# Performance work log

Measured on AMD Instinct MI355X. Metric: run time of the kernel, lower is better.

## Reference

```python
import jax, jax.numpy as jnp
import numpy as np

N, E, H, L = 50000, 600000, 128, 4  # nodes, edges, hidden_dim, num_layers


def setup_inputs() -> dict:
    key = jax.random.key(0)
    ks = jax.random.split(key, 12)
    def w(k, shape):
        fan_in = shape[-2]
        return jax.random.normal(k, shape, jnp.float32) / np.float32(np.sqrt(fan_in))
    return {
        "loc": jax.random.normal(ks[0], (N, 3), jnp.float32),
        "vel": jax.random.normal(ks[1], (N, 3), jnp.float32),
        "edge_attr": jax.random.normal(ks[2], (E, 2), jnp.float32),
        "row": jax.random.randint(ks[3], (E,), 0, N),
        "col": jax.random.randint(ks[4], (E,), 0, N),
        # embedding: Linear(6 -> H)
        "emb_w": w(ks[5], (6, H)), "emb_b": jnp.zeros((H,), jnp.float32),
        # per-layer edge MLP: Linear(2H+2 -> H), SiLU, Linear(H -> H), SiLU
        "ew1": w(ks[6], (L, 2 * H + 2, H)), "eb1": jnp.zeros((L, H), jnp.float32),
        "ew2": w(ks[7], (L, H, H)), "eb2": jnp.zeros((L, H), jnp.float32),
        # per-layer node MLP: Linear(2H -> H), SiLU, Linear(H -> H)
        "nw1": w(ks[8], (L, 2 * H, H)), "nb1": jnp.zeros((L, H), jnp.float32),
        "nw2": w(ks[9], (L, H, H)), "nb2": jnp.zeros((L, H), jnp.float32),
        # decoder: Linear(H -> H), SiLU, Linear(H -> 3)
        "dw1": w(ks[10], (H, H)), "db1": jnp.zeros((H,), jnp.float32),
        "dw2": w(ks[11], (H, 3)), "db2": jnp.zeros((3,), jnp.float32),
    }


def reference(loc, vel, edge_attr, row, col, emb_w, emb_b, ew1, eb1, ew2, eb2,
              nw1, nb1, nw2, nb2, dw1, db1, dw2, db2):
    silu = jax.nn.silu
    # embedding of [loc, vel]
    h = jnp.concatenate([loc, vel], axis=1) @ emb_w + emb_b  # [N, H]
    for i in range(L):
        # edge model: gather endpoints, concat edge_attr, 2-layer SiLU MLP
        e_in = jnp.concatenate([h[row], h[col], edge_attr], axis=1)  # [E, 2H+2]
        m = silu(silu(e_in @ ew1[i] + eb1[i]) @ ew2[i] + eb2[i])     # [E, H]
        # node model: scatter-sum messages into source nodes (row), MLP, residual
        agg = jax.ops.segment_sum(m, row, num_segments=N)            # [N, H]
        upd = silu(jnp.concatenate([h, agg], axis=1) @ nw1[i] + nb1[i]) @ nw2[i] + nb2[i]
        h = h + upd  # recurrent=True
    return silu(h @ dw1 + db1) @ dw2 + db2  # [N, 3]
```

## Files before the change

kernel.cpp:

```cpp
#include <hip/hip_runtime.h>

#define NN 50000
#define NE 600000
#define HD 128
#define NL 4
#define NSCB 196
#define NWG_E (NE/64)

typedef __bf16 bf16x8 __attribute__((ext_vector_type(8)));
typedef float f32x4 __attribute__((ext_vector_type(4)));

__device__ __forceinline__ unsigned short f2bf(float x){
  union { float f; unsigned int u; } v; v.f = x;
  unsigned int r = v.u + 0x7FFFu + ((v.u >> 16) & 1u);
  return (unsigned short)(r >> 16);
}
__device__ __forceinline__ float silu_f(float x){
  float e, r;
  float t = x * -1.44269504088896340736f;
  asm("v_exp_f32 %0, %1" : "=v"(e) : "v"(t));
  float d = 1.f + e;
  asm("v_rcp_f32 %0, %1" : "=v"(r) : "v"(d));
  return x * r;
}
__device__ __forceinline__ unsigned pk_bf16(float v0, float v1){
  unsigned r;
  asm("v_cvt_pk_bf16_f32 %0, %1, %2" : "=v"(r) : "v"(v0), "v"(v1));
  return r;
}
__device__ __forceinline__ void atomic_pk_add_bf16(unsigned short* addr, unsigned data){
  asm volatile("global_atomic_pk_add_bf16 %0, %1, off"
    :: "v"((unsigned long long)(uintptr_t)addr), "v"(data) : "memory");
}

__device__ __forceinline__ f32x4 mfma_b16(bf16x8 a, bf16x8 b, f32x4 c){
  return __builtin_amdgcn_mfma_f32_16x16x32_bf16(a, b, c, 0, 0, 0);
}

typedef __attribute__((address_space(1))) const unsigned int* gas1p;
typedef __attribute__((address_space(3))) unsigned int* las3p;
__device__ __forceinline__ void gll16(const void* g, void* l){
  __builtin_amdgcn_global_load_lds((gas1p)g, (las3p)l, 16, 0, 0);
}

__global__ __launch_bounds__(256) void pack_b(const float* __restrict__ src,
    unsigned short* __restrict__ dst, int K, int Klimit, int srcLayerStride, int perm){
  int layer = blockIdx.y;
  int tid = blockIdx.x*256 + threadIdx.x;
  int j = tid & 7, lane = (tid >> 3) & 63, nb = (tid >> 9) & 7, kk = tid >> 12;
  int krow = (kk << 5) + ((lane >> 4) << 3) + j;
  int ll = lane & 15;
  int c = perm ? (((((nb >> 1) << 4) + ll) << 1) + (nb & 1)) : ((nb << 4) + ll);
  float v = (krow < Klimit) ? src[(size_t)layer*srcLayerStride + krow*HD + c] : 0.f;
  dst[(size_t)layer*K*HD + tid] = f2bf(v);
}

__global__ __launch_bounds__(256) void emb_kernel(
    const float* __restrict__ loc, const float* __restrict__ vel,
    const float* __restrict__ ew, const float* __restrict__ eb,
    float* __restrict__ hf, unsigned short* __restrict__ hb)
{
  int gid = blockIdx.x*256 + threadIdx.x;
  int n = gid >> 7, j = gid & 127;
  float s = eb[j];
  s += loc[n*3+0]*ew[0*HD+j] + loc[n*3+1]*ew[1*HD+j] + loc[n*3+2]*ew[2*HD+j];
  s += vel[n*3+0]*ew[3*HD+j] + vel[n*3+1]*ew[4*HD+j] + vel[n*3+2]*ew[5*HD+j];
  hf[gid] = s;
  hb[gid] = f2bf(s);
}

__global__ __launch_bounds__(256) void count_kernel(const int* __restrict__ rowIdx, int* __restrict__ cnt){
  int e = blockIdx.x*256 + threadIdx.x;
  if (e < NE) atomicAdd(cnt + rowIdx[e], 1);
}

__global__ __launch_bounds__(256) void blocksum_kernel(const int* __restrict__ cnt, int* __restrict__ bsum){
  __shared__ int s[256];
  int t = threadIdx.x, i = blockIdx.x*256 + t;
  s[t] = (i < NN) ? cnt[i] : 0;
  __syncthreads();
  for (int d = 128; d > 0; d >>= 1){
    if (t < d) s[t] += s[t + d];
    __syncthreads();
  }
  if (t == 0) bsum[blockIdx.x] = s[0];
}

__global__ __launch_bounds__(256) void scanb_kernel(int* __restrict__ bsum){
  __shared__ int s[256];
  int t = threadIdx.x;
  int v = (t < NSCB) ? bsum[t] : 0;
  s[t] = v;
  __syncthreads();
  for (int d = 1; d < 256; d <<= 1){
    int u = (t >= d) ? s[t-d] : 0;
    __syncthreads();
    s[t] += u;
    __syncthreads();
  }
  if (t < NSCB) bsum[t] = s[t] - v;
}

__global__ __launch_bounds__(256) void offsets_kernel(const int* __restrict__ cnt,
    const int* __restrict__ bsum, int* __restrict__ cur){
  __shared__ int s[256];
  int t = threadIdx.x, i = blockIdx.x*256 + t;
  int v = (i < NN) ? cnt[i] : 0;
  s[t] = v;
  __syncthreads();
  for (int d = 1; d < 256; d <<= 1){
    int u = (t >= d) ? s[t-d] : 0;
    __syncthreads();
    s[t] += u;
    __syncthreads();
  }
  if (i < NN) cur[i] = bsum[blockIdx.x] + s[t] - v;
}

__global__ __launch_bounds__(256) void assign_kernel(
    const int* __restrict__ rowIdx, const int* __restrict__ colIdx,
    const float* __restrict__ ea, int* __restrict__ cur,
    int* __restrict__ row_s, int* __restrict__ col_s, float* __restrict__ ea_s){
  int e = blockIdx.x*256 + threadIdx.x;
  if (e < NE){
    int r = rowIdx[e];
    int s = atomicAdd(cur + r, 1);
    int s64 = s & 63;
    int sp = (s & ~63) | (((s64 >> 2) & 3) << 4) | (((s64 >> 4) & 3) << 2) | (s64 & 3);
    row_s[sp] = r;
    col_s[sp] = colIdx[e];
    ea_s[2*sp]   = ea[2*e];
    ea_s[2*sp+1] = ea[2*e+1];
  }
}

#define SWZ(a) ((a) ^ (((a) >> 4) & 0x30))

__global__ __launch_bounds__(256, 8) void edge_kernel(
    const unsigned short* __restrict__ hb,
    const int* __restrict__ row_s, const int* __restrict__ col_s,
    const float* __restrict__ ea_s,
    const unsigned short* __restrict__ B1p, const unsigned short* __restrict__ B2p,
    const float* __restrict__ bias1, const float* __restrict__ bias2,
    const float* __restrict__ wea,
    unsigned short* __restrict__ aggb)
{
  __shared__ alignas(128) char sA[1024*16];
  __shared__ int sRow[64];
  __shared__ float2 sEa[64];
  uint4* sA4 = reinterpret_cast<uint4*>(sA);

  const int t = threadIdx.x;
  const int w = t >> 6, l = t & 63, lw = l >> 4, ll = l & 15;

  int orig = blockIdx.x;
  int xcd = orig & 7, idx = orig >> 3;
  const int qq = NWG_E >> 3, rr = NWG_E & 7;
  int bid = (xcd < rr) ? xcd*(qq + 1) + idx : rr*(qq + 1) + (xcd - rr)*qq + idx;
  const int e0 = bid << 6;

  if (t < 64){
    sRow[t] = row_s[e0 + t];
    sEa[t] = reinterpret_cast<const float2*>(ea_s)[e0 + t];
  }
  const int er = e0 + (w << 4) + ll;
  const int nrow = row_s[er];
  const int ncol = col_s[er];
  const unsigned short* gr = hb + (size_t)nrow*HD + (lw << 3);
  #pragma unroll
  for (int kk = 0; kk < 4; ++kk)
    gll16(gr + (kk << 5), sA + ((size_t)(((kk << 2) + w)) << 10));
  asm volatile("s_waitcnt vmcnt(0)" ::: "memory");
  __syncthreads();

  const int q2 = ((w << 4) + ll) << 1;
  const float2 bb1 = *reinterpret_cast<const float2*>(bias1 + q2);
  const float2 wA = *reinterpret_cast<const float2*>(wea + q2);
  const float2 wB = *reinterpret_cast<const float2*>(wea + HD + q2);

  f32x4 acc[4][2] = {};
  #pragma unroll
  for (int kk = 0; kk < 4; ++kk){
    bf16x8 a[4], b[2];
    #pragma unroll
    for (int r = 0; r < 4; ++r)
      a[r] = *reinterpret_cast<const bf16x8*>(&sA4[((kk << 2) + r)*64 + l]);
    #pragma unroll
    for (int c = 0; c < 2; ++c)
      b[c] = *reinterpret_cast<const bf16x8*>(B1p + ((((kk << 3) + (w << 1) + c) << 6) + l)*8);
    #pragma unroll
    for (int r = 0; r < 4; ++r)
      #pragma unroll
      for (int c = 0; c < 2; ++c)
        acc[r][c] = mfma_b16(a[r], b[c], acc[r][c]);
  }
  __syncthreads();

  const unsigned short* gc = hb + (size_t)ncol*HD + (lw << 3);
  #pragma unroll
  for (int kk = 0; kk < 4; ++kk)
    gll16(gc + (kk << 5), sA + ((size_t)(((kk << 2) + w)) << 10));
  asm volatile("s_waitcnt vmcnt(0)" ::: "memory");
  __syncthreads();

  #pragma unroll
  for (int kk = 4; kk < 8; ++kk){
    bf16x8 a[4], b[2];
    #pragma unroll
    for (int r = 0; r < 4; ++r)
      a[r] = *reinterpret_cast<const bf16x8*>(&sA4[(((kk - 4) << 2) + r)*64 + l]);
    #pragma unroll
    for (int c = 0; c < 2; ++c)
      b[c] = *reinterpret_cast<const bf16x8*>(B1p + ((((kk << 3) + (w << 1) + c) << 6) + l)*8);
    #pragma unroll
    for (int r = 0; r < 4; ++r)
      #pragma unroll
      for (int c = 0; c < 2; ++c)
        acc[r][c] = mfma_b16(a[r], b[c], acc[r][c]);
  }
  __syncthreads();

  #pragma unroll
  for (int r = 0; r < 4; ++r){
    #pragma unroll
    for (int i = 0; i < 4; ++i){
      int rt = (r << 4) + (lw << 2) + i;
      float2 eav = sEa[rt];
      float v0 = silu_f(acc[r][0][i] + bb1.x + eav.x*wA.x + eav.y*wB.x);
      float v1 = silu_f(acc[r][1][i] + bb1.y + eav.x*wA.y + eav.y*wB.y);
      unsigned d = pk_bf16(v0, v1);
      int a0 = ((((w << 2) + r) << 10) | ((ll >> 2) << 8) | (lw << 6) | (i << 4) | ((ll & 3) << 2));
      *reinterpret_cast<unsigned*>(sA + SWZ(a0)) = d;
    }
  }
  __syncthreads();

  f32x4 acc2[4][2] = {};
  #pragma unroll
  for (int kk = 0; kk < 4; ++kk){
    bf16x8 a[4], b[2];
    #pragma unroll
    for (int r = 0; r < 4; ++r){
      int a0 = ((((kk << 2) + r) << 10) | (l << 4));
      a[r] = *reinterpret_cast<const bf16x8*>(sA + SWZ(a0));
    }
    #pragma unroll
    for (int c = 0; c < 2; ++c)
      b[c] = *reinterpret_cast<const bf16x8*>(B2p + ((((kk << 3) + (w << 1) + c) << 6) + l)*8);
    #pragma unroll
    for (int r = 0; r < 4; ++r)
      #pragma unroll
      for (int c = 0; c < 2; ++c)
        acc2[r][c] = mfma_b16(a[r], b[c], acc2[r][c]);
  }

  {
    const float2 bb2 = *reinterpret_cast<const float2*>(bias2 + q2);
    int curNode = -1;
    float s0 = 0.f, s1 = 0.f;
    #pragma unroll
    for (int r = 0; r < 4; ++r){
      #pragma unroll
      for (int i = 0; i < 4; ++i){
        int rt = (r << 4) + (lw << 2) + i;
        int nd = sRow[rt];
        float v0 = silu_f(acc2[r][0][i] + bb2.x);
        float v1 = silu_f(acc2[r][1][i] + bb2.y);
        if (nd != curNode){
          if (curNode >= 0)
            atomic_pk_add_bf16(aggb + (size_t)curNode*HD + q2, pk_bf16(s0, s1));
          curNode = nd; s0 = v0; s1 = v1;
        } else { s0 += v0; s1 += v1; }
      }
    }
    atomic_pk_add_bf16(aggb + (size_t)curNode*HD + q2, pk_bf16(s0, s1));
  }
}

__global__ __launch_bounds__(256, 8) void node_kernel(
    unsigned short* hb, unsigned short* aggb,
    const unsigned short* __restrict__ B1p, const unsigned short* __restrict__ B2p,
    const float* __restrict__ bias1, const float* __restrict__ bias2,
    float* hf)
{
  __shared__ alignas(128) char sA[1024*16];
  uint4* sA4 = reinterpret_cast<uint4*>(sA);
  const int t = threadIdx.x;
  const int w = t >> 6, l = t & 63, lw = l >> 4, ll = l & 15;
  const int n0 = blockIdx.x << 6;

  const int nlane = n0 + (w << 4) + ll;
  const int ncl = (nlane < NN) ? nlane : 0;
  const unsigned short* gh = hb + (size_t)ncl*HD + (lw << 3);
  #pragma unroll
  for (int kk = 0; kk < 4; ++kk)
    gll16(gh + (kk << 5), sA + ((size_t)(((kk << 2) + w)) << 10));
  asm volatile("s_waitcnt vmcnt(0)" ::: "memory");
  __syncthreads();

  const int q2 = ((w << 4) + ll) << 1;
  const float2 bb1 = *reinterpret_cast<const float2*>(bias1 + q2);

  f32x4 acc[4][2] = {};
  #pragma unroll
  for (int kk = 0; kk < 4; ++kk){
    bf16x8 a[4], b[2];
    #pragma unroll
    for (int r = 0; r < 4; ++r)
      a[r] = *reinterpret_cast<const bf16x8*>(&sA4[((kk << 2) + r)*64 + l]);
    #pragma unroll
    for (int c = 0; c < 2; ++c)
      b[c] = *reinterpret_cast<const bf16x8*>(B1p + ((((kk << 3) + (w << 1) + c) << 6) + l)*8);
    #pragma unroll
    for (int r = 0; r < 4; ++r)
      #pragma unroll
      for (int c = 0; c < 2; ++c)
        acc[r][c] = mfma_b16(a[r], b[c], acc[r][c]);
  }
  __syncthreads();

  unsigned short* ga = aggb + (size_t)ncl*HD + (lw << 3);
  #pragma unroll
  for (int kk = 0; kk < 4; ++kk)
    gll16(ga + (kk << 5), sA + ((size_t)(((kk << 2) + w)) << 10));
  asm volatile("s_waitcnt vmcnt(0)" ::: "memory");
  if (nlane < NN){
    const uint4 z4 = make_uint4(0u, 0u, 0u, 0u);
    #pragma unroll
    for (int kk = 0; kk < 4; ++kk)
      *reinterpret_cast<uint4*>(ga + (kk << 5)) = z4;
  }
  __syncthreads();

  #pragma unroll
  for (int kk = 4; kk < 8; ++kk){
    bf16x8 a[4], b[2];
    #pragma unroll
    for (int r = 0; r < 4; ++r)
      a[r] = *reinterpret_cast<const bf16x8*>(&sA4[(((kk - 4) << 2) + r)*64 + l]);
    #pragma unroll
    for (int c = 0; c < 2; ++c)
      b[c] = *reinterpret_cast<const bf16x8*>(B1p + ((((kk << 3) + (w << 1) + c) << 6) + l)*8);
    #pragma unroll
    for (int r = 0; r < 4; ++r)
      #pragma unroll
      for (int c = 0; c < 2; ++c)
        acc[r][c] = mfma_b16(a[r], b[c], acc[r][c]);
  }
  __syncthreads();

  #pragma unroll
  for (int r = 0; r < 4; ++r){
    #pragma unroll
    for (int i = 0; i < 4; ++i){
      unsigned d = pk_bf16(silu_f(acc[r][0][i] + bb1.x), silu_f(acc[r][1][i] + bb1.y));
      int a0 = ((((w << 2) + r) << 10) | ((ll >> 2) << 8) | (lw << 6) | (i << 4) | ((ll & 3) << 2));
      *reinterpret_cast<unsigned*>(sA + SWZ(a0)) = d;
    }
  }
  __syncthreads();

  f32x4 acc2[4][2] = {};
  #pragma unroll
  for (int kk = 0; kk < 4; ++kk){
    bf16x8 a[4], b[2];
    #pragma unroll
    for (int r = 0; r < 4; ++r){
      int a0 = ((((kk << 2) + r) << 10) | (l << 4));
      a[r] = *reinterpret_cast<const bf16x8*>(sA + SWZ(a0));
    }
    #pragma unroll
    for (int c = 0; c < 2; ++c)
      b[c] = *reinterpret_cast<const bf16x8*>(B2p + ((((kk << 3) + (w << 1) + c) << 6) + l)*8);
    #pragma unroll
    for (int r = 0; r < 4; ++r)
      #pragma unroll
      for (int c = 0; c < 2; ++c)
        acc2[r][c] = mfma_b16(a[r], b[c], acc2[r][c]);
  }

  {
    const float2 bb2 = *reinterpret_cast<const float2*>(bias2 + q2);
    #pragma unroll
    for (int r = 0; r < 4; ++r){
      #pragma unroll
      for (int i = 0; i < 4; ++i){
        int rt = (r << 4) + (lw << 2) + i;
        int n = n0 + rt;
        if (n < NN){
          float2 ho = *reinterpret_cast<const float2*>(hf + (size_t)n*HD + q2);
          float h0 = ho.x + acc2[r][0][i] + bb2.x;
          float h1 = ho.y + acc2[r][1][i] + bb2.y;
          *reinterpret_cast<float2*>(hf + (size_t)n*HD + q2) = make_float2(h0, h1);
          *reinterpret_cast<unsigned*>(hb + (size_t)n*HD + q2) = pk_bf16(h0, h1);
        }
      }
    }
  }
}

__global__ __launch_bounds__(256) void dec_kernel(
    const unsigned short* __restrict__ hb, const unsigned short* __restrict__ D1p,
    const float* __restrict__ db1, const float* __restrict__ dw2,
    const float* __restrict__ db2, float* __restrict__ outp)
{
  __shared__ alignas(128) char sA[1024*16];
  uint4* sA4 = reinterpret_cast<uint4*>(sA);
  __shared__ float sT[64*133];
  const int t = threadIdx.x;
  const int n0 = blockIdx.x << 6;
  {
    const int nl_ = t >> 2, p = t & 3;
    const int n = n0 + nl_;
    const bool valid = (n < NN);
    const int nc = valid ? n : 0;
    const uint4* src = reinterpret_cast<const uint4*>(hb + (size_t)nc*HD);
    const int base16 = ((nl_ >> 4) << 6) + (nl_ & 15);
    #pragma unroll
    for (int c = 0; c < 4; ++c){
      int q = (p << 2) + c;
      uint4 d = valid ? src[q] : make_uint4(0,0,0,0);
      sA4[base16 + ((q >> 2) << 8) + ((q & 3) << 4)] = d;
    }
  }
  __syncthreads();

  const int w = t >> 6, l = t & 63;
  const int lw = l >> 4, ll = l & 15;

  f32x4 acc[4][2] = {};
  #pragma unroll
  for (int kk = 0; kk < 4; ++kk){
    bf16x8 a[4], b[2];
    #pragma unroll
    for (int r = 0; r < 4; ++r)
      a[r] = *reinterpret_cast<const bf16x8*>(&sA4[((kk << 2) + r)*64 + l]);
    #pragma unroll
    for (int c = 0; c < 2; ++c)
      b[c] = *reinterpret_cast<const bf16x8*>(D1p + ((((kk << 3) + (w << 1) + c) << 6) + l)*8);
    #pragma unroll
    for (int r = 0; r < 4; ++r)
      #pragma unroll
      for (int c = 0; c < 2; ++c)
        acc[r][c] = mfma_b16(a[r], b[c], acc[r][c]);
  }
  #pragma unroll
  for (int r = 0; r < 4; ++r){
    #pragma unroll
    for (int i = 0; i < 4; ++i){
      int rt = (r << 4) + (lw << 2) + i;
      #pragma unroll
      for (int c = 0; c < 2; ++c){
        int col = (w << 5) + (c << 4) + ll;
        sT[rt*133 + col] = silu_f(acc[r][c][i] + db1[col]);
      }
    }
  }
  __syncthreads();
  if (t < 192){
    int rr = t & 63, cc = t >> 6;
    int n = n0 + rr;
    if (n < NN){
      float s = db2[cc];
      #pragma unroll 8
      for (int k = 0; k < HD; ++k) s += sT[rr*133 + k]*dw2[k*3 + cc];
      outp[(size_t)n*3 + cc] = s;
    }
  }
}

static inline char* alignup(char* p, size_t a){ return (char*)(((uintptr_t)p + a - 1) & ~(a - 1)); }

extern "C" void kernel_launch(void* const* d_in, const int* in_sizes, int n_in,
                              void* d_out, int out_size, void* d_ws, size_t ws_size,
                              hipStream_t stream)
{
  const float* loc  = (const float*)d_in[0];
  const float* vel  = (const float*)d_in[1];
  const float* ea   = (const float*)d_in[2];
  const int*   row  = (const int*)d_in[3];
  const int*   col  = (const int*)d_in[4];
  const float* embw = (const float*)d_in[5];
  const float* embb = (const float*)d_in[6];
  const float* ew1  = (const float*)d_in[7];
  const float* eb1  = (const float*)d_in[8];
  const float* ew2  = (const float*)d_in[9];
  const float* eb2  = (const float*)d_in[10];
  const float* nw1  = (const float*)d_in[11];
  const float* nb1  = (const float*)d_in[12];
  const float* nw2  = (const float*)d_in[13];
  const float* nb2  = (const float*)d_in[14];
  const float* dw1  = (const float*)d_in[15];
  const float* db1  = (const float*)d_in[16];
  const float* dw2  = (const float*)d_in[17];
  const float* db2  = (const float*)d_in[18];

  char* p = (char*)d_ws;
  float* hf = (float*)p;                       p += (size_t)NN*HD*4;
  unsigned short* hbuf = (unsigned short*)p;   p += (size_t)NN*HD*2;
  unsigned short* aggb = (unsigned short*)p;   p += (size_t)NN*HD*2;
  int* cnt = (int*)p;                          p += (size_t)NN*4;
  int* cur = (int*)p;                          p += (size_t)NN*4;
  int* bsum = (int*)p;                         p += (size_t)256*4;   p = alignup(p, 256);
  int* row_s = (int*)p;                        p += (size_t)NE*4;
  int* col_s = (int*)p;                        p += (size_t)NE*4;
  float* ea_s = (float*)p;                     p += (size_t)NE*2*4;
  unsigned short* ew1p = (unsigned short*)p;   p += (size_t)NL*256*HD*2;
  unsigned short* ew2p = (unsigned short*)p;   p += (size_t)NL*128*HD*2;
  unsigned short* nw1p = (unsigned short*)p;   p += (size_t)NL*256*HD*2;
  unsigned short* nw2p = (unsigned short*)p;   p += (size_t)NL*128*HD*2;
  unsigned short* dw1p = (unsigned short*)p;   p += (size_t)128*HD*2;

  hipMemsetAsync(cnt, 0, (size_t)NN*4, stream);
  count_kernel<<<(NE + 255)/256, 256, 0, stream>>>(row, cnt);
  blocksum_kernel<<<NSCB, 256, 0, stream>>>(cnt, bsum);
  scanb_kernel<<<1, 256, 0, stream>>>(bsum);
  offsets_kernel<<<NSCB, 256, 0, stream>>>(cnt, bsum, cur);
  assign_kernel<<<(NE + 255)/256, 256, 0, stream>>>(row, col, ea, cur, row_s, col_s, ea_s);

  pack_b<<<dim3(128, NL), 256, 0, stream>>>(ew1, ew1p, 256, 256, 258*HD, 1);
  pack_b<<<dim3(64,  NL), 256, 0, stream>>>(ew2, ew2p, 128, 128, 128*HD, 1);
  pack_b<<<dim3(128, NL), 256, 0, stream>>>(nw1, nw1p, 256, 256, 256*HD, 1);
  pack_b<<<dim3(64,  NL), 256, 0, stream>>>(nw2, nw2p, 128, 128, 128*HD, 1);
  pack_b<<<dim3(64,  1 ), 256, 0, stream>>>(dw1, dw1p, 128, 128, 0, 0);

  emb_kernel<<<(NN*HD)/256, 256, 0, stream>>>(loc, vel, embw, embb, hf, hbuf);

  hipMemsetAsync(aggb, 0, (size_t)NN*HD*2, stream);
  for (int i = 0; i < NL; ++i){
    edge_kernel<<<NWG_E, 256, 0, stream>>>(hbuf, row_s, col_s, ea_s,
        ew1p + (size_t)i*256*HD, ew2p + (size_t)i*128*HD,
        eb1 + i*HD, eb2 + i*HD,
        ew1 + (size_t)i*258*HD + 256*HD, aggb);
    node_kernel<<<(NN + 63)/64, 256, 0, stream>>>(hbuf, aggb,
        nw1p + (size_t)i*256*HD, nw2p + (size_t)i*128*HD,
        nb1 + i*HD, nb2 + i*HD, hf);
  }

  dec_kernel<<<(NN + 63)/64, 256, 0, stream>>>(hbuf, dw1p, db1, dw2, db2, (float*)d_out);
}
```

Baseline: 586.5 us.

## Process two edge tiles per workgroup and prefetch next row gather during scatter

Each edge-kernel workgroup now handles two consecutive 64-edge tiles instead of one, halving the grid. The row-endpoint gather for the second tile is issued into shared memory before the first tile's atomic scatter, so its memory latency can hide behind the atomics. The XCD block remapping is simplified to fit the new grid size. The trade-off is fewer workgroups for latency hiding. The vmcnt(0) wait also waits on the outstanding atomics, which may limit the overlap.

```diff
diff --git a/kernel.cpp b/kernel.cpp
--- a/kernel.cpp
+++ b/kernel.cpp
@@ -5,7 +5,8 @@
 #define HD 128
 #define NL 4
 #define NSCB 196
-#define NWG_E (NE/64)
+#define NTILE 9375
+#define NWG_E2 4688
 
 typedef __bf16 bf16x8 __attribute__((ext_vector_type(8)));
 typedef float f32x4 __attribute__((ext_vector_type(4)));
@@ -146,134 +147,162 @@
     unsigned short* __restrict__ aggb)
 {
   __shared__ alignas(128) char sA[1024*16];
-  __shared__ int sRow[64];
-  __shared__ float2 sEa[64];
+  __shared__ int sRow[2][64];
+  __shared__ float2 sEa[2][64];
   uint4* sA4 = reinterpret_cast<uint4*>(sA);
 
   const int t = threadIdx.x;
   const int w = t >> 6, l = t & 63, lw = l >> 4, ll = l & 15;
 
-  int orig = blockIdx.x;
-  int xcd = orig & 7, idx = orig >> 3;
-  const int qq = NWG_E >> 3, rr = NWG_E & 7;
-  int bid = (xcd < rr) ? xcd*(qq + 1) + idx : rr*(qq + 1) + (xcd - rr)*qq + idx;
-  const int e0 = bid << 6;
-
-  if (t < 64){
-    sRow[t] = row_s[e0 + t];
-    sEa[t] = reinterpret_cast<const float2*>(ea_s)[e0 + t];
-  }
-  const int er = e0 + (w << 4) + ll;
-  const int nrow = row_s[er];
-  const int ncol = col_s[er];
-  const unsigned short* gr = hb + (size_t)nrow*HD + (lw << 3);
-  #pragma unroll
-  for (int kk = 0; kk < 4; ++kk)
-    gll16(gr + (kk << 5), sA + ((size_t)(((kk << 2) + w)) << 10));
-  asm volatile("s_waitcnt vmcnt(0)" ::: "memory");
+  const int orig = blockIdx.x;
+  const int bid = (orig & 7)*586 + (orig >> 3);
+  const int tile0 = bid << 1;
+
+  {
+    const int e0 = tile0 << 6;
+    if (t < 64){
+      sRow[0][t] = row_s[e0 + t];
+      sEa[0][t] = reinterpret_cast<const float2*>(ea_s)[e0 + t];
+    }
+    const int er = e0 + (w << 4) + ll;
+    const unsigned short* gr = hb + (size_t)row_s[er]*HD + (lw << 3);
+    #pragma unroll
+    for (int kk = 0; kk < 4; ++kk)
+      gll16(gr + (kk << 5), sA + ((size_t)(((kk << 2) + w)) << 10));
+    asm volatile("s_waitcnt vmcnt(0)" ::: "memory");
+  }
   __syncthreads();
 
   const int q2 = ((w << 4) + ll) << 1;
   const float2 bb1 = *reinterpret_cast<const float2*>(bias1 + q2);
   const float2 wA = *reinterpret_cast<const float2*>(wea + q2);
   const float2 wB = *reinterpret_cast<const float2*>(wea + HD + q2);
-
-  f32x4 acc[4][2] = {};
-  #pragma unroll
-  for (int kk = 0; kk < 4; ++kk){
-    bf16x8 a[4], b[2];
-    #pragma unroll
-    for (int r = 0; r < 4; ++r)
-      a[r] = *reinterpret_cast<const bf16x8*>(&sA4[((kk << 2) + r)*64 + l]);
-    #pragma unroll
-    for (int c = 0; c < 2; ++c)
-      b[c] = *reinterpret_cast<const bf16x8*>(B1p + ((((kk << 3) + (w << 1) + c) << 6) + l)*8);
-    #pragma unroll
-    for (int r = 0; r < 4; ++r)
-      #pragma unroll
-      for (int c = 0; c < 2; ++c)
-        acc[r][c] = mfma_b16(a[r], b[c], acc[r][c]);
-  }
-  __syncthreads();
-
-  const unsigned short* gc = hb + (size_t)ncol*HD + (lw << 3);
-  #pragma unroll
-  for (int kk = 0; kk < 4; ++kk)
-    gll16(gc + (kk << 5), sA + ((size_t)(((kk << 2) + w)) << 10));
-  asm volatile("s_waitcnt vmcnt(0)" ::: "memory");
-  __syncthreads();
-
-  #pragma unroll
-  for (int kk = 4; kk < 8; ++kk){
-    bf16x8 a[4], b[2];
-    #pragma unroll
-    for (int r = 0; r < 4; ++r)
-      a[r] = *reinterpret_cast<const bf16x8*>(&sA4[(((kk - 4) << 2) + r)*64 + l]);
-    #pragma unroll
-    for (int c = 0; c < 2; ++c)
-      b[c] = *reinterpret_cast<const bf16x8*>(B1p + ((((kk << 3) + (w << 1) + c) << 6) + l)*8);
-    #pragma unroll
-    for (int r = 0; r < 4; ++r)
-      #pragma unroll
-      for (int c = 0; c < 2; ++c)
-        acc[r][c] = mfma_b16(a[r], b[c], acc[r][c]);
-  }
-  __syncthreads();
-
-  #pragma unroll
-  for (int r = 0; r < 4; ++r){
-    #pragma unroll
-    for (int i = 0; i < 4; ++i){
-      int rt = (r << 4) + (lw << 2) + i;
-      float2 eav = sEa[rt];
-      float v0 = silu_f(acc[r][0][i] + bb1.x + eav.x*wA.x + eav.y*wB.x);
-      float v1 = silu_f(acc[r][1][i] + bb1.y + eav.x*wA.y + eav.y*wB.y);
-      unsigned d = pk_bf16(v0, v1);
-      int a0 = ((((w << 2) + r) << 10) | ((ll >> 2) << 8) | (lw << 6) | (i << 4) | ((ll & 3) << 2));
-      *reinterpret_cast<unsigned*>(sA + SWZ(a0)) = d;
-    }
-  }
-  __syncthreads();
-
-  f32x4 acc2[4][2] = {};
-  #pragma unroll
-  for (int kk = 0; kk < 4; ++kk){
-    bf16x8 a[4], b[2];
-    #pragma unroll
-    for (int r = 0; r < 4; ++r){
-      int a0 = ((((kk << 2) + r) << 10) | (l << 4));
-      a[r] = *reinterpret_cast<const bf16x8*>(sA + SWZ(a0));
-    }
-    #pragma unroll
-    for (int c = 0; c < 2; ++c)
-      b[c] = *reinterpret_cast<const bf16x8*>(B2p + ((((kk << 3) + (w << 1) + c) << 6) + l)*8);
-    #pragma unroll
-    for (int r = 0; r < 4; ++r)
-      #pragma unroll
-      for (int c = 0; c < 2; ++c)
-        acc2[r][c] = mfma_b16(a[r], b[c], acc2[r][c]);
-  }
-
-  {
-    const float2 bb2 = *reinterpret_cast<const float2*>(bias2 + q2);
-    int curNode = -1;
-    float s0 = 0.f, s1 = 0.f;
+  const float2 bb2 = *reinterpret_cast<const float2*>(bias2 + q2);
+
+  #pragma unroll
+  for (int hh = 0; hh < 2; ++hh){
+    const int tile = tile0 + hh;
+    const int erh = (tile << 6) + (w << 4) + ll;
+
+    f32x4 acc[4][2] = {};
+    #pragma unroll
+    for (int kk = 0; kk < 4; ++kk){
+      bf16x8 a[4], b[2];
+      #pragma unroll
+      for (int r = 0; r < 4; ++r)
+        a[r] = *reinterpret_cast<const bf16x8*>(&sA4[((kk << 2) + r)*64 + l]);
+      #pragma unroll
+      for (int c = 0; c < 2; ++c)
+        b[c] = *reinterpret_cast<const bf16x8*>(B1p + ((((kk << 3) + (w << 1) + c) << 6) + l)*8);
+      #pragma unroll
+      for (int r = 0; r < 4; ++r)
+        #pragma unroll
+        for (int c = 0; c < 2; ++c)
+          acc[r][c] = mfma_b16(a[r], b[c], acc[r][c]);
+    }
+    __syncthreads();
+
+    {
+      const unsigned short* gc = hb + (size_t)col_s[erh]*HD + (lw << 3);
+      #pragma unroll
+      for (int kk = 0; kk < 4; ++kk)
+        gll16(gc + (kk << 5), sA + ((size_t)(((kk << 2) + w)) << 10));
+      asm volatile("s_waitcnt vmcnt(0)" ::: "memory");
+    }
+    __syncthreads();
+
+    #pragma unroll
+    for (int kk = 4; kk < 8; ++kk){
+      bf16x8 a[4], b[2];
+      #pragma unroll
+      for (int r = 0; r < 4; ++r)
+        a[r] = *reinterpret_cast<const bf16x8*>(&sA4[(((kk - 4) << 2) + r)*64 + l]);
+      #pragma unroll
+      for (int c = 0; c < 2; ++c)
+        b[c] = *reinterpret_cast<const bf16x8*>(B1p + ((((kk << 3) + (w << 1) + c) << 6) + l)*8);
+      #pragma unroll
+      for (int r = 0; r < 4; ++r)
+        #pragma unroll
+        for (int c = 0; c < 2; ++c)
+          acc[r][c] = mfma_b16(a[r], b[c], acc[r][c]);
+    }
+    __syncthreads();
+
     #pragma unroll
     for (int r = 0; r < 4; ++r){
       #pragma unroll
       for (int i = 0; i < 4; ++i){
         int rt = (r << 4) + (lw << 2) + i;
-        int nd = sRow[rt];
-        float v0 = silu_f(acc2[r][0][i] + bb2.x);
-        float v1 = silu_f(acc2[r][1][i] + bb2.y);
-        if (nd != curNode){
-          if (curNode >= 0)
-            atomic_pk_add_bf16(aggb + (size_t)curNode*HD + q2, pk_bf16(s0, s1));
-          curNode = nd; s0 = v0; s1 = v1;
-        } else { s0 += v0; s1 += v1; }
+        float2 eav = sEa[hh][rt];
+        float v0 = silu_f(acc[r][0][i] + bb1.x + eav.x*wA.x + eav.y*wB.x);
+        float v1 = silu_f(acc[r][1][i] + bb1.y + eav.x*wA.y + eav.y*wB.y);
+        unsigned d = pk_bf16(v0, v1);
+        int a0 = ((((w << 2) + r) << 10) | ((ll >> 2) << 8) | (lw << 6) | (i << 4) | ((ll & 3) << 2));
+        *reinterpret_cast<unsigned*>(sA + SWZ(a0)) = d;
       }
     }
-    atomic_pk_add_bf16(aggb + (size_t)curNode*HD + q2, pk_bf16(s0, s1));
+    __syncthreads();
+
+    f32x4 acc2[4][2] = {};
+    #pragma unroll
+    for (int kk = 0; kk < 4; ++kk){
+      bf16x8 a[4], b[2];
+      #pragma unroll
+      for (int r = 0; r < 4; ++r){
+        int a0 = ((((kk << 2) + r) << 10) | (l << 4));
+        a[r] = *reinterpret_cast<const bf16x8*>(sA + SWZ(a0));
+      }
+      #pragma unroll
+      for (int c = 0; c < 2; ++c)
+        b[c] = *reinterpret_cast<const bf16x8*>(B2p + ((((kk << 3) + (w << 1) + c) << 6) + l)*8);
+      #pragma unroll
+      for (int r = 0; r < 4; ++r)
+        #pragma unroll
+        for (int c = 0; c < 2; ++c)
+          acc2[r][c] = mfma_b16(a[r], b[c], acc2[r][c]);
+    }
+    __syncthreads();
+
+    const bool more = (hh == 0) && (tile0 + 1 < NTILE);
+    if (more){
+      const int e1 = (tile0 + 1) << 6;
+      if (t < 64){
+        sRow[1][t] = row_s[e1 + t];
+        sEa[1][t] = reinterpret_cast<const float2*>(ea_s)[e1 + t];
+      }
+      const int er1 = e1 + (w << 4) + ll;
+      const unsigned short* gr1 = hb + (size_t)row_s[er1]*HD + (lw << 3);
+      #pragma unroll
+      for (int kk = 0; kk < 4; ++kk)
+        gll16(gr1 + (kk << 5), sA + ((size_t)(((kk << 2) + w)) << 10));
+    }
+
+    {
+      int curNode = -1;
+      float s0 = 0.f, s1 = 0.f;
+      #pragma unroll
+      for (int r = 0; r < 4; ++r){
+        #pragma unroll
+        for (int i = 0; i < 4; ++i){
+          int rt = (r << 4) + (lw << 2) + i;
+          int nd = sRow[hh][rt];
+          float v0 = silu_f(acc2[r][0][i] + bb2.x);
+          float v1 = silu_f(acc2[r][1][i] + bb2.y);
+          if (nd != curNode){
+            if (curNode >= 0)
+              atomic_pk_add_bf16(aggb + (size_t)curNode*HD + q2, pk_bf16(s0, s1));
+            curNode = nd; s0 = v0; s1 = v1;
+          } else { s0 += v0; s1 += v1; }
+        }
+      }
+      atomic_pk_add_bf16(aggb + (size_t)curNode*HD + q2, pk_bf16(s0, s1));
+    }
+
+    if (hh == 0){
+      if (!more) return;
+      asm volatile("s_waitcnt vmcnt(0)" ::: "memory");
+      __syncthreads();
+    }
   }
 }
 
@@ -528,7 +557,7 @@
 
   hipMemsetAsync(aggb, 0, (size_t)NN*HD*2, stream);
   for (int i = 0; i < NL; ++i){
-    edge_kernel<<<NWG_E, 256, 0, stream>>>(hbuf, row_s, col_s, ea_s,
+    edge_kernel<<<NWG_E2, 256, 0, stream>>>(hbuf, row_s, col_s, ea_s,
         ew1p + (size_t)i*256*HD, ew2p + (size_t)i*128*HD,
         eb1 + i*HD, eb2 + i*HD,
         ew1 + (size_t)i*258*HD + 256*HD, aggb);
```

Measured after the change: 869.0 us. 48.2% more time.
